# Kernel tuning notes

Hardware: AMD Instinct MI355X
Metric: run time of the kernel (lower is better)

The kernel has to match this reference:

```python
import jax, jax.numpy as jnp
import numpy as np

RENDER_STEP = 0.005
N_FREQS = 6

def pos_enc(x):
    # x: [N,3] -> [N, 3 + 2*N_FREQS*3]
    freqs = (2.0 ** jnp.arange(N_FREQS, dtype=x.dtype)) * jnp.pi
    xb = x[:, None, :] * freqs[:, None]            # [N,F,3]
    enc = jnp.concatenate([jnp.sin(xb), jnp.cos(xb)], axis=-1).reshape(x.shape[0], -1)
    return jnp.concatenate([x, enc], axis=-1)

def geom_fwd(points, Wg0, bg0, Wg1, bg1, Wg2, bg2):
    h = jax.nn.relu(pos_enc(points) @ Wg0 + bg0)
    h = jax.nn.relu(h @ Wg1 + bg1)
    return h @ Wg2 + bg2                           # [N,16]; ch0 = sdf, full vec = features


def setup_inputs() -> dict:
    key = jax.random.key(0)
    ks = jax.random.split(key, 12)
    n_rays, n_samples = 16384, 524288
    sc = lambda fan_in: 1.0 / np.sqrt(fan_in)
    inp = {
        'rays_o': jax.random.normal(ks[0], (n_rays, 3), jnp.float32) * 0.5,
        'rays_d': jax.random.normal(ks[1], (n_rays, 3), jnp.float32),
        'ray_indices': jnp.sort(jax.random.randint(ks[2], (n_samples,), 0, n_rays, jnp.int32)),
        't_starts': jax.random.uniform(ks[3], (n_samples, 1), jnp.float32),
        'random_points': jax.random.normal(ks[4], (1024, 3), jnp.float32),
        's_var': jnp.ones((1,), jnp.float32),
        'Wg0': jax.random.normal(ks[5], (39, 256), jnp.float32) * sc(39),
        'bg0': jnp.zeros((256,), jnp.float32),
        'Wg1': jax.random.normal(ks[6], (256, 256), jnp.float32) * sc(256),
        'bg1': jnp.zeros((256,), jnp.float32),
        'Wg2': jax.random.normal(ks[7], (256, 16), jnp.float32) * sc(256),
        'bg2': jnp.zeros((16,), jnp.float32),
        'Wc0': jax.random.normal(ks[8], (25, 256), jnp.float32) * sc(25),
        'bc0': jnp.zeros((256,), jnp.float32),
        'Wc1': jax.random.normal(ks[9], (256, 3), jnp.float32) * sc(256),
        'bc1': jnp.zeros((3,), jnp.float32),
    }
    return inp


def reference(rays_o, rays_d, ray_indices, t_starts, random_points, s_var,
              Wg0, bg0, Wg1, bg1, Wg2, bg2, Wc0, bc0, Wc1, bc1):
    n_rays = rays_o.shape[0]
    rays_d = rays_d / (jnp.linalg.norm(rays_d, axis=-1, keepdims=True) + 1e-10)

    midpoints = t_starts + RENDER_STEP * 0.5       # [N,1]
    t_intervals = RENDER_STEP
    t_origins = rays_o[ray_indices]                # gather [N,3]
    t_dirs = rays_d[ray_indices]
    points = t_origins + t_dirs * midpoints        # [N,3]

    # SDF network forward + analytic gradient wrt points (one fwd + one bwd)
    out, vjp_fn = jax.vjp(lambda p: geom_fwd(p, Wg0, bg0, Wg1, bg1, Wg2, bg2), points)
    sdf = out[:, 0]                                # [N]
    feats = out                                    # [N,16]
    cot = jnp.zeros_like(out).at[:, 0].set(1.0)
    grad = vjp_fn(cot)[0]                          # dSDF/dpoints [N,3]
    normal = grad / (jnp.linalg.norm(grad, axis=-1, keepdims=True) + 1e-10)

    # color network: dirs + feats + points + normal -> rgb
    cin = jnp.concatenate([t_dirs, feats, points, normal], axis=-1)   # [N,25]
    rgbs = jax.nn.sigmoid(jax.nn.relu(cin @ Wc0 + bc0) @ Wc1 + bc1)   # [N,3]

    # get_alpha (cos_anneal_ratio = 1.0)
    inv_s = jnp.clip(jnp.exp(s_var[0]), 1e-6, 1e6)
    dSDF_dt = jnp.sum(grad * t_dirs, axis=-1, keepdims=True)
    dSDF_dt = -jax.nn.relu(-dSDF_dt)
    cdf = jax.nn.sigmoid(inv_s * sdf[:, None])
    rho = jnp.maximum(inv_s * (cdf - 1.0) * dSDF_dt, 0.0)
    alpha = 1.0 - jnp.exp(-rho * t_intervals)      # [N,1]

    # render_weight_from_alpha: per-ray exclusive cumprod of (1-alpha), log-space
    a = jnp.clip(alpha[:, 0], 0.0, 1.0 - 1e-7)
    loga = jnp.log1p(-a)
    E = jnp.cumsum(loga) - loga                    # exclusive cumsum
    starts = jnp.clip(jnp.searchsorted(ray_indices, jnp.arange(n_rays, dtype=ray_indices.dtype)),
                      0, a.shape[0] - 1)           # first sample idx per ray
    trans = jnp.exp(E - E[starts][ray_indices])    # per-ray transmittance
    weights = (a * trans)[:, None]                 # [N,1]

    seg = lambda v: jax.ops.segment_sum(weights * v, ray_indices, num_segments=n_rays)
    opacity = jax.ops.segment_sum(weights, ray_indices, num_segments=n_rays)  # [R,1]
    depth = seg(midpoints)
    pixels_color = seg(rgbs)
    pixels_normal = seg(normal)
    pixels_normal = pixels_normal / (jnp.linalg.norm(pixels_normal, axis=-1, keepdims=True) + 1e-10)

    random_sdfs = geom_fwd(random_points, Wg0, bg0, Wg1, bg1, Wg2, bg2)[:, :1]
    return (pixels_color, pixels_normal, opacity, depth, weights, sdf, random_sdfs)
```

## Files before the change

### kernel.cpp

```cpp
#include <hip/hip_runtime.h>
#include <math.h>


#define TILE 32
#define NTHREADS 512
#define LDP 264
#define LDE 56
#define LDCIN 40
#define PI_F 3.14159265358979323846f

typedef _Float16 half8 __attribute__((ext_vector_type(8)));
typedef float f32x4 __attribute__((ext_vector_type(4)));
typedef float f32x16 __attribute__((ext_vector_type(16)));

struct alignas(16) SMemK2 {
    _Float16 a0h[TILE * LDP];
    _Float16 a0l[TILE * LDP];
    _Float16 a1h[TILE * LDP];
    _Float16 a1l[TILE * LDP];
    _Float16 ench[TILE * LDE];
    _Float16 encl[TILE * LDE];
    float feats[TILE * 16];
    float red1 [TILE * 16];
    float pts [TILE * 4];
    float dirs[TILE * 4];
    float nrm [TILE * 4];
};

__device__ __forceinline__ void splitst(float v, _Float16* ph, _Float16* pl) {
    _Float16 h = (_Float16)v;
    *ph = h;
    *pl = (_Float16)(v - (float)h);
}

__device__ __forceinline__ f32x16 zero16() {
    f32x16 z;
#pragma unroll
    for (int i = 0; i < 16; ++i) z[i] = 0.f;
    return z;
}

template<int KITERS, bool BIAS, bool RELU, bool AMASK, bool CMASK, bool WLO>
__device__ __forceinline__ void gemm32(
    const _Float16* Ah, const _Float16* Al, const int lda,
    const _Float16* __restrict__ Bp, const float* __restrict__ bias,
    _Float16* Ch, _Float16* Cl, const int ldc,
    const int lane, const int nt)
{
    f32x16 acc0 = zero16(), acc1 = zero16();
    const int row  = lane & 31;
    const int koff = (lane >> 5) * 8;
    const _Float16* ahb = Ah + row * lda + koff;
    const _Float16* alb = Al + row * lda + koff;
    const _Float16* bbase = Bp + ((size_t)nt * KITERS * 64 + lane) * 16;

    half8 ax[2], ay[2];
    half8 bh[3], bl[3];
    ax[0] = *(const half8*)ahb;
    if (!AMASK) ay[0] = *(const half8*)alb;
    bh[0] = *(const half8*)bbase;
    if (!AMASK) bl[0] = *(const half8*)(bbase + 8);
    if (KITERS > 1) {
        bh[1] = *(const half8*)(bbase + 1024);
        if (!AMASK) bl[1] = *(const half8*)(bbase + 1024 + 8);
    }

#pragma unroll
    for (int kit = 0; kit < KITERS; ++kit) {
        const int ac = kit & 1, an = ac ^ 1;
        const int bc = kit % 3;
        if (kit + 1 < KITERS) {
            ax[an] = *(const half8*)(ahb + (kit + 1) * 16);
            if (!AMASK) ay[an] = *(const half8*)(alb + (kit + 1) * 16);
        }
        if (kit + 2 < KITERS) {
            const int bn = (kit + 2) % 3;
            const _Float16* bp = bbase + (size_t)(kit + 2) * 1024;
            bh[bn] = *(const half8*)bp;
            if (!AMASK) bl[bn] = *(const half8*)(bp + 8);
        }
        f32x16& acc = ac ? acc1 : acc0;
        if (AMASK) {
            half8 m;
#pragma unroll
            for (int j = 0; j < 8; ++j) {
                _Float16 t = ax[ac][j] * (_Float16)16384.f;
                m[j] = (t < (_Float16)1.f) ? t : (_Float16)1.f;
            }
            __builtin_amdgcn_s_setprio(1);
            acc = __builtin_amdgcn_mfma_f32_32x32x16_f16(m, bh[bc], acc, 0, 0, 0);
            __builtin_amdgcn_s_setprio(0);
        } else {
            __builtin_amdgcn_s_setprio(1);
            acc = __builtin_amdgcn_mfma_f32_32x32x16_f16(ay[ac], bh[bc], acc, 0, 0, 0);
            acc = __builtin_amdgcn_mfma_f32_32x32x16_f16(ax[ac], bl[bc], acc, 0, 0, 0);
            acc = __builtin_amdgcn_mfma_f32_32x32x16_f16(ax[ac], bh[bc], acc, 0, 0, 0);
            __builtin_amdgcn_s_setprio(0);
        }
    }
    const int col = lane & 31;
    const int rb  = (lane >> 5) * 4;
    const int jc  = nt * 32 + col;
    const float bs = BIAS ? bias[jc] : 0.f;
#pragma unroll
    for (int r = 0; r < 16; ++r) {
        const int srow = (r & 3) + 8 * (r >> 2) + rb;
        float v = acc0[r] + acc1[r] + bs;
        if (RELU) v = (v > 0.f) ? fmaxf(v, 1e-4f) : 0.f;
        if (CMASK) { if (!((float)Ch[srow * ldc + jc] > 0.f)) v = 0.f; }
        _Float16 h = (_Float16)v;
        Ch[srow * ldc + jc] = h;
        if (WLO) Cl[srow * ldc + jc] = (_Float16)(v - (float)h);
    }
}

template<int KITERS>
__device__ __forceinline__ void gemm16(
    const _Float16* Ah, const _Float16* Al, const int lda,
    const _Float16* __restrict__ Bp,
    _Float16* Ch, _Float16* Cl, const int ldc,
    const int lane, const int mt, const int ntbase)
{
    f32x4 acc0 = (f32x4){0.f,0.f,0.f,0.f}, acc1 = (f32x4){0.f,0.f,0.f,0.f};
    const int m  = mt * 16 + (lane & 15);
    const int q8 = (lane >> 4) * 8;
    const _Float16* ahb = Ah + m * lda + q8;
    const _Float16* alb = Al + m * lda + q8;
    const _Float16* bbase = Bp + ((size_t)ntbase * KITERS * 64 + lane) * 16;

    half8 ax[2], ay[2], bh[3], bl[3];
    ax[0] = *(const half8*)ahb;
    ay[0] = *(const half8*)alb;
    bh[0] = *(const half8*)bbase;
    bl[0] = *(const half8*)(bbase + 8);
    if (KITERS > 1) {
        bh[1] = *(const half8*)(bbase + 1024);
        bl[1] = *(const half8*)(bbase + 1024 + 8);
    }
#pragma unroll
    for (int kit = 0; kit < KITERS; ++kit) {
        const int ac = kit & 1, an = ac ^ 1;
        const int bc = kit % 3;
        if (kit + 1 < KITERS) {
            ax[an] = *(const half8*)(ahb + (kit + 1) * 32);
            ay[an] = *(const half8*)(alb + (kit + 1) * 32);
        }
        if (kit + 2 < KITERS) {
            const int bn = (kit + 2) % 3;
            const _Float16* bp = bbase + (size_t)(kit + 2) * 1024;
            bh[bn] = *(const half8*)bp;
            bl[bn] = *(const half8*)(bp + 8);
        }
        f32x4& acc = ac ? acc1 : acc0;
        __builtin_amdgcn_s_setprio(1);
        acc = __builtin_amdgcn_mfma_f32_16x16x32_f16(ay[ac], bh[bc], acc, 0, 0, 0);
        acc = __builtin_amdgcn_mfma_f32_16x16x32_f16(ax[ac], bl[bc], acc, 0, 0, 0);
        acc = __builtin_amdgcn_mfma_f32_16x16x32_f16(ax[ac], bh[bc], acc, 0, 0, 0);
        __builtin_amdgcn_s_setprio(0);
    }
    const int col = lane & 15, q = lane >> 4;
    const int j = ntbase * 16 + col;
#pragma unroll
    for (int r = 0; r < 4; ++r) {
        const int s = mt * 16 + q * 4 + r;
        float v = acc0[r] + acc1[r];
        _Float16 h = (_Float16)v;
        Ch[s * ldc + j] = h;
        Cl[s * ldc + j] = (_Float16)(v - (float)h);
    }
}

__device__ __forceinline__ void kpartial16(
    const _Float16* Ah, const _Float16* Al,
    const _Float16* __restrict__ Bp,
    float* red0, float* red1, const int lane, const int w)
{
    const int mt = w & 1, ks = w >> 1;
    const int m  = mt * 16 + (lane & 15);
    const int q8 = (lane >> 4) * 8;
    const _Float16* ahb = Ah + m * LDP + q8 + ks * 128;
    const _Float16* alb = Al + m * LDP + q8 + ks * 128;
    const _Float16* bbase = Bp + ((size_t)(ks * 4) * 64 + lane) * 16;
    f32x4 acc0 = (f32x4){0.f,0.f,0.f,0.f}, acc1 = (f32x4){0.f,0.f,0.f,0.f};
#pragma unroll
    for (int kit = 0; kit < 4; ++kit) {
        half8 a = *(const half8*)(ahb + kit * 32);
        half8 y = *(const half8*)(alb + kit * 32);
        const _Float16* bp = bbase + (size_t)kit * 1024;
        half8 bh = *(const half8*)bp;
        half8 bl = *(const half8*)(bp + 8);
        f32x4& acc = (kit & 1) ? acc1 : acc0;
        __builtin_amdgcn_s_setprio(1);
        acc = __builtin_amdgcn_mfma_f32_16x16x32_f16(y, bh, acc, 0, 0, 0);
        acc = __builtin_amdgcn_mfma_f32_16x16x32_f16(a, bl, acc, 0, 0, 0);
        acc = __builtin_amdgcn_mfma_f32_16x16x32_f16(a, bh, acc, 0, 0, 0);
        __builtin_amdgcn_s_setprio(0);
    }
    float* red = ks ? red1 : red0;
    const int col = lane & 15, q = lane >> 4;
#pragma unroll
    for (int r = 0; r < 4; ++r)
        red[(mt * 16 + q * 4 + r) * 16 + col] += acc0[r] + acc1[r];
}

__global__ __launch_bounds__(256) void k0_pack(
    const float* __restrict__ Wg0, const float* __restrict__ Wg1,
    const float* __restrict__ Wg2, const float* __restrict__ Wc0,
    const float* __restrict__ Wc1,
    _Float16* __restrict__ Wg0p, _Float16* __restrict__ Wg1p,
    _Float16* __restrict__ Wg1Tp, _Float16* __restrict__ Wg0Tp,
    _Float16* __restrict__ Wc0p, _Float16* __restrict__ Wg2p,
    _Float16* __restrict__ Wc1p)
{
    int gid = blockIdx.x * 256 + threadIdx.x;
    if (gid >= 176128) return;
    int idx, kiters, mode;
    _Float16* dst;
    if      (gid <  12288) { idx = gid;          kiters = 3;  dst = Wg0p;  mode = 0; }
    else if (gid <  77824) { idx = gid -  12288; kiters = 16; dst = Wg1p;  mode = 1; }
    else if (gid < 143360) { idx = gid -  77824; kiters = 16; dst = Wg1Tp; mode = 2; }
    else if (gid < 159744) { idx = gid - 143360; kiters = 8;  dst = Wg0Tp; mode = 3; }
    else if (gid < 167936) { idx = gid - 159744; kiters = 2;  dst = Wc0p;  mode = 4; }
    else if (gid < 172032) { idx = gid - 167936; kiters = 8;  dst = Wg2p;  mode = 5; }
    else                   { idx = gid - 172032; kiters = 8;  dst = Wc1p;  mode = 6; }
    const bool p32 = (mode == 0 || mode == 1 || mode == 2 || mode == 4);
    int j = idx & 7, lane = (idx >> 3) & 63, rest = idx >> 9;
    int kit = rest % kiters, nt = rest / kiters;
    int k, n;
    if (p32) { k = kit * 16 + ((lane >> 5) << 3) + j; n = (nt << 5) + (lane & 31); }
    else     { k = kit * 32 + ((lane >> 4) << 3) + j; n = (nt << 4) + (lane & 15); }
    float val = 0.f;
    switch (mode) {
        case 0: val = (k < 39) ? Wg0[k * 256 + n] : 0.f; break;
        case 1: val = Wg1[k * 256 + n]; break;
        case 2: val = Wg1[n * 256 + k] * Wg2[k * 16]; break;
        case 3: val = (n < 39) ? Wg0[n * 256 + k] : 0.f; break;
        case 4: val = (k < 25) ? Wc0[k * 256 + n] : 0.f; break;
        case 5: val = Wg2[k * 16 + n]; break;
        case 6: val = (n < 3) ? Wc1[k * 3 + n] : 0.f; break;
    }
    _Float16 h = (_Float16)val;
    _Float16 l = (_Float16)(val - (float)h);
    int off = ((nt * kiters + kit) * 64 + lane) * 16 + j;
    dst[off] = h;
    dst[off + 8] = l;
}

__global__ __launch_bounds__(512, 4) void k2_mlp(
    const float* __restrict__ rays_o, const float* __restrict__ rays_d,
    const int*   __restrict__ ray_idx, const float* __restrict__ t_starts,
    const float* __restrict__ s_var,
    const float* __restrict__ bg0, const float* __restrict__ bg1,
    const float* __restrict__ bg2,
    const float* __restrict__ bc0, const float* __restrict__ bc1,
    const _Float16* __restrict__ Wg0p, const _Float16* __restrict__ Wg1p,
    const _Float16* __restrict__ Wg1Tp, const _Float16* __restrict__ Wg0Tp,
    const _Float16* __restrict__ Wc0p, const _Float16* __restrict__ Wg2p,
    const _Float16* __restrict__ Wc1p,
    float* __restrict__ out_sdf, float* __restrict__ ws_a,
    float* __restrict__ ws_rgb, float* __restrict__ ws_nrm,
    int Nsamp)
{
    __shared__ SMemK2 sm;
    const int tid = threadIdx.x;
    const int lane = tid & 63;
    const int w = tid >> 6;
    const int n0 = blockIdx.x * TILE;

    for (int i = tid; i < TILE * 16; i += NTHREADS) {
        sm.feats[i] = bg2[i & 15];
        sm.red1[i] = 0.f;
    }
    if (tid < TILE) {
        int n = n0 + tid; if (n >= Nsamp) n = Nsamp - 1;
        int ri = ray_idx[n];
        float dx = rays_d[ri * 3 + 0], dy = rays_d[ri * 3 + 1], dz = rays_d[ri * 3 + 2];
        float inv = 1.f / (sqrtf(dx * dx + dy * dy + dz * dz) + 1e-10f);
        dx *= inv; dy *= inv; dz *= inv;
        float mid = t_starts[n] + 0.0025f;
        sm.dirs[tid * 4 + 0] = dx; sm.dirs[tid * 4 + 1] = dy; sm.dirs[tid * 4 + 2] = dz;
        float px = rays_o[ri * 3 + 0] + dx * mid;
        float py = rays_o[ri * 3 + 1] + dy * mid;
        float pz = rays_o[ri * 3 + 2] + dz * mid;
        sm.pts[tid * 4 + 0] = px; sm.pts[tid * 4 + 1] = py; sm.pts[tid * 4 + 2] = pz;
        splitst(px, &sm.ench[tid * LDE + 0], &sm.encl[tid * LDE + 0]);
        splitst(py, &sm.ench[tid * LDE + 1], &sm.encl[tid * LDE + 1]);
        splitst(pz, &sm.ench[tid * LDE + 2], &sm.encl[tid * LDE + 2]);
    }
    __syncthreads();

    for (int i = tid; i < TILE * 3; i += NTHREADS) {
        int s = i & 31;
        int d = i >> 5;
        float x = sm.pts[s * 4 + d];
        float a = PI_F * x;
        float sv = sinf(a), cv = cosf(a);
#pragma unroll
        for (int f = 0; f < 6; ++f) {
            splitst(sv, &sm.ench[s * LDE + 3 + f * 6 + d],     &sm.encl[s * LDE + 3 + f * 6 + d]);
            splitst(cv, &sm.ench[s * LDE + 3 + f * 6 + 3 + d], &sm.encl[s * LDE + 3 + f * 6 + 3 + d]);
            float s2 = 2.f * sv * cv;
            float c2 = 1.f - 2.f * sv * sv;
            sv = s2; cv = c2;
        }
    }
    for (int i = tid; i < TILE * 9; i += NTHREADS) {
        int s = i / 9, c = 39 + (i - s * 9);
        sm.ench[s * LDE + c] = (_Float16)0.f;
        sm.encl[s * LDE + c] = (_Float16)0.f;
    }
    __syncthreads();

    gemm32<3, true, true, false, false, true>(sm.ench, sm.encl, LDE,
                                              Wg0p, bg0, sm.a0h, sm.a0l, LDP, lane, w);
    __syncthreads();

    gemm32<16, true, true, false, false, true>(sm.a0h, sm.a0l, LDP,
                                               Wg1p, bg1, sm.a1h, sm.a1l, LDP, lane, w);
    __syncthreads();

    if (w < 4)
        kpartial16(sm.a1h, sm.a1l, Wg2p, sm.feats, sm.red1, lane, w);

    gemm32<16, false, false, true, true, true>(sm.a1h, sm.a1l, LDP,
                                               Wg1Tp, nullptr, sm.a0h, sm.a0l, LDP, lane, w);
    __syncthreads();

    if (w < 6)
        gemm16<8>(sm.a0h, sm.a0l, LDP, Wg0Tp,
                  sm.a1h, sm.a1l, LDP, lane, w & 1, w >> 1);
    __syncthreads();

    if (tid < TILE) {
        int s = tid;
        float g[3];
#pragma unroll
        for (int d = 0; d < 3; ++d)
            g[d] = (float)sm.a1h[s * LDP + d] + (float)sm.a1l[s * LDP + d];
#pragma unroll
        for (int f = 0; f < 6; ++f) {
            float freq = PI_F * (float)(1 << f);
#pragma unroll
            for (int d = 0; d < 3; ++d) {
                int cs = 3 + f * 6 + d, cc = cs + 3;
                float gs = (float)sm.a1h[s * LDP + cs] + (float)sm.a1l[s * LDP + cs];
                float gc = (float)sm.a1h[s * LDP + cc] + (float)sm.a1l[s * LDP + cc];
                float sv = (float)sm.ench[s * LDE + cs] + (float)sm.encl[s * LDE + cs];
                float cv = (float)sm.ench[s * LDE + cc] + (float)sm.encl[s * LDE + cc];
                g[d] += freq * (gs * cv - gc * sv);
            }
        }
        float gl = sqrtf(g[0] * g[0] + g[1] * g[1] + g[2] * g[2]);
        float invl = 1.f / (gl + 1e-10f);
        float nx = g[0] * invl, ny = g[1] * invl, nz = g[2] * invl;
        sm.nrm[s * 4 + 0] = nx; sm.nrm[s * 4 + 1] = ny; sm.nrm[s * 4 + 2] = nz;
        float dx = sm.dirs[s * 4 + 0], dy = sm.dirs[s * 4 + 1], dz = sm.dirs[s * 4 + 2];
        float dsdt = fminf(g[0] * dx + g[1] * dy + g[2] * dz, 0.f);
        float sdf = sm.feats[s * 16 + 0] + sm.red1[s * 16 + 0];
        float inv_s = __expf(s_var[0]);
        inv_s = fminf(fmaxf(inv_s, 1e-6f), 1e6f);
        float cdf = 1.f / (1.f + __expf(-inv_s * sdf));
        float rho = fmaxf(inv_s * (cdf - 1.f) * dsdt, 0.f);
        float alpha = 1.f - __expf(-rho * 0.005f);
        float a = fminf(fmaxf(alpha, 0.f), 1.f - 1e-7f);
        int n = n0 + s;
        if (n < Nsamp) {
            out_sdf[n] = sdf;
            ws_a[n] = a;
            ws_nrm[n * 3 + 0] = nx; ws_nrm[n * 3 + 1] = ny; ws_nrm[n * 3 + 2] = nz;
        }
    }
    __syncthreads();

    _Float16* cinh = sm.a0h;
    _Float16* cinl = sm.a0l;
    for (int i = tid; i < TILE * 32; i += NTHREADS) {
        int s = i >> 5, c = i & 31;
        float v = 0.f;
        if      (c < 3)  v = sm.dirs[s * 4 + c];
        else if (c < 19) v = sm.feats[s * 16 + (c - 3)] + sm.red1[s * 16 + (c - 3)];
        else if (c < 22) v = sm.pts[s * 4 + (c - 19)];
        else if (c < 25) v = sm.nrm[s * 4 + (c - 22)];
        splitst(v, &cinh[s * LDCIN + c], &cinl[s * LDCIN + c]);
    }
    __syncthreads();

    for (int i = tid; i < TILE * 16; i += NTHREADS) {
        sm.feats[i] = ((i & 15) < 3) ? bc1[i & 15] : 0.f;
        sm.red1[i] = 0.f;
    }

    gemm32<2, true, true, false, false, true>(cinh, cinl, LDCIN,
                                              Wc0p, bc0, sm.a1h, sm.a1l, LDP, lane, w);
    __syncthreads();

    if (w < 4)
        kpartial16(sm.a1h, sm.a1l, Wc1p, sm.feats, sm.red1, lane, w);
    __syncthreads();

    if (tid < TILE) {
        int n = n0 + tid;
        if (n < Nsamp) {
#pragma unroll
            for (int c = 0; c < 3; ++c) {
                float z = sm.feats[tid * 16 + c] + sm.red1[tid * 16 + c];
                ws_rgb[n * 3 + c] = 1.f / (1.f + __expf(-z));
            }
        }
    }
}

__global__ void k3_composite(
    const int* __restrict__ ray_idx, const float* __restrict__ t_starts,
    const float* __restrict__ ws_a, const float* __restrict__ ws_rgb,
    const float* __restrict__ ws_nrm,
    float* __restrict__ out_pc, float* __restrict__ out_pn,
    float* __restrict__ out_op, float* __restrict__ out_dp,
    float* __restrict__ out_w, int n_rays, int Nsamp)
{
    int r = blockIdx.x * blockDim.x + threadIdx.x;
    if (r >= n_rays) return;
    int lo = 0, hi = Nsamp;
    while (lo < hi) { int m = (lo + hi) >> 1; if (ray_idx[m] < r) lo = m + 1; else hi = m; }
    int start = lo;
    hi = Nsamp;
    while (lo < hi) { int m = (lo + hi) >> 1; if (ray_idx[m] < r + 1) lo = m + 1; else hi = m; }
    int end = lo;

    float T = 1.f, aco = 0.f, acd = 0.f;
    float c0 = 0.f, c1 = 0.f, c2 = 0.f, nx = 0.f, ny = 0.f, nz = 0.f;
    for (int n = start; n < end; ++n) {
        float a = ws_a[n];
        float wgt = a * T;
        T *= (1.f - a);
        out_w[n] = wgt;
        float mid = t_starts[n] + 0.0025f;
        aco += wgt; acd += wgt * mid;
        c0 += wgt * ws_rgb[n * 3 + 0];
        c1 += wgt * ws_rgb[n * 3 + 1];
        c2 += wgt * ws_rgb[n * 3 + 2];
        nx += wgt * ws_nrm[n * 3 + 0];
        ny += wgt * ws_nrm[n * 3 + 1];
        nz += wgt * ws_nrm[n * 3 + 2];
    }
    out_op[r] = aco;
    out_dp[r] = acd;
    out_pc[r * 3 + 0] = c0; out_pc[r * 3 + 1] = c1; out_pc[r * 3 + 2] = c2;
    float nl = sqrtf(nx * nx + ny * ny + nz * nz);
    float inv = 1.f / (nl + 1e-10f);
    out_pn[r * 3 + 0] = nx * inv; out_pn[r * 3 + 1] = ny * inv; out_pn[r * 3 + 2] = nz * inv;
}

__global__ __launch_bounds__(256) void k4_random(
    const float* __restrict__ pts,
    const float* __restrict__ Wg0, const float* __restrict__ bg0,
    const float* __restrict__ Wg1, const float* __restrict__ bg1,
    const float* __restrict__ Wg2, const float* __restrict__ bg2,
    float* __restrict__ out_rs, int n_rand)
{
    __shared__ float enc[40];
    __shared__ float h[256];
    __shared__ float red[256];
    int b = blockIdx.x;
    if (b >= n_rand) return;
    int tid = threadIdx.x;
    if (tid < 39) {
        int c = tid;
        float v;
        if (c < 3) v = pts[b * 3 + c];
        else {
            int e = c - 3, f = e / 6, r = e - f * 6;
            float freq = PI_F * (float)(1 << f);
            int d = (r < 3) ? r : r - 3;
            float x = pts[b * 3 + d];
            v = (r < 3) ? sinf(freq * x) : cosf(freq * x);
        }
        enc[c] = v;
    }
    __syncthreads();
    {
        float z = bg0[tid];
        for (int m = 0; m < 39; ++m) z += enc[m] * Wg0[m * 256 + tid];
        h[tid] = fmaxf(z, 0.f);
    }
    __syncthreads();
    {
        float z = bg1[tid];
        for (int k = 0; k < 256; ++k) z += h[k] * Wg1[k * 256 + tid];
        float h1 = fmaxf(z, 0.f);
        red[tid] = h1 * Wg2[tid * 16];
    }
    __syncthreads();
    for (int off = 128; off > 0; off >>= 1) {
        if (tid < off) red[tid] += red[tid + off];
        __syncthreads();
    }
    if (tid == 0) out_rs[b] = red[0] + bg2[0];
}

extern "C" void kernel_launch(void* const* d_in, const int* in_sizes, int n_in,
                              void* d_out, int out_size, void* d_ws, size_t ws_size,
                              hipStream_t stream)
{
    const float* rays_o   = (const float*)d_in[0];
    const float* rays_d   = (const float*)d_in[1];
    const int*   ray_idx  = (const int*)  d_in[2];
    const float* t_starts = (const float*)d_in[3];
    const float* rpts     = (const float*)d_in[4];
    const float* s_var    = (const float*)d_in[5];
    const float* Wg0 = (const float*)d_in[6];  const float* bg0 = (const float*)d_in[7];
    const float* Wg1 = (const float*)d_in[8];  const float* bg1 = (const float*)d_in[9];
    const float* Wg2 = (const float*)d_in[10]; const float* bg2 = (const float*)d_in[11];
    const float* Wc0 = (const float*)d_in[12]; const float* bc0 = (const float*)d_in[13];
    const float* Wc1 = (const float*)d_in[14]; const float* bc1 = (const float*)d_in[15];

    const int n_rays = in_sizes[0] / 3;
    const int Ns     = in_sizes[2];
    const int n_rand = in_sizes[4] / 3;

    float* out  = (float*)d_out;
    float* o_pc = out;
    float* o_pn = out + (size_t)3 * n_rays;
    float* o_op = out + (size_t)6 * n_rays;
    float* o_dp = out + (size_t)7 * n_rays;
    float* o_w  = out + (size_t)8 * n_rays;
    float* o_sdf = o_w + Ns;
    float* o_rs  = o_sdf + Ns;

    _Float16* hptr  = (_Float16*)d_ws;
    _Float16* Wg0p  = hptr;
    _Float16* Wg1p  = Wg0p  + 24576;
    _Float16* Wg1Tp = Wg1p  + 131072;
    _Float16* Wg0Tp = Wg1Tp + 131072;
    _Float16* Wc0p  = Wg0Tp + 32768;
    _Float16* Wg2p  = Wc0p  + 16384;
    _Float16* Wc1p  = Wg2p  + 8192;
    float* fbase  = (float*)(hptr + 352256);
    float* ws_a   = fbase;
    float* ws_rgb = ws_a + Ns;
    float* ws_nrm = ws_rgb + (size_t)3 * Ns;

    hipLaunchKernelGGL(k0_pack, dim3(688), dim3(256), 0, stream,
                       Wg0, Wg1, Wg2, Wc0, Wc1,
                       Wg0p, Wg1p, Wg1Tp, Wg0Tp, Wc0p, Wg2p, Wc1p);
    hipLaunchKernelGGL(k2_mlp, dim3((Ns + TILE - 1) / TILE), dim3(NTHREADS), 0, stream,
                       rays_o, rays_d, ray_idx, t_starts, s_var,
                       bg0, bg1, bg2, bc0, bc1,
                       Wg0p, Wg1p, Wg1Tp, Wg0Tp, Wc0p, Wg2p, Wc1p,
                       o_sdf, ws_a, ws_rgb, ws_nrm, Ns);
    hipLaunchKernelGGL(k4_random, dim3(n_rand), dim3(256), 0, stream,
                       rpts, Wg0, bg0, Wg1, bg1, Wg2, bg2, o_rs, n_rand);
    hipLaunchKernelGGL(k3_composite, dim3((n_rays + 255) / 256), dim3(256), 0, stream,
                       ray_idx, t_starts, ws_a, ws_rgb, ws_nrm,
                       o_pc, o_pn, o_op, o_dp, o_w, n_rays, Ns);
}
```

Baseline: 729.4 us.

## Fold random-point SDF into MLP kernel and parallelize compositing per-ray wavefront

Random-point SDF evaluation now runs as extra tiles of the tensor-core MLP kernel, which exit after the SDF head, replacing the separate scalar k4_random kernel. The compositing kernel assigns one 64-lane wavefront per ray and computes transmittance with a shuffle-based prefix product, replacing one serial thread per ray. Points are recomputed directly in the encoding loop and normals are written straight into the color-input tile, which removes one barrier and a shared buffer. The risks are extra redundant gathers, and wasted lanes in the compositing kernel, since rays average about 32 samples and each wavefront still runs two binary searches.

```diff
diff --git a/kernel.cpp b/kernel.cpp
--- a/kernel.cpp
+++ b/kernel.cpp
@@ -24,7 +24,6 @@
     float red1 [TILE * 16];
     float pts [TILE * 4];
     float dirs[TILE * 4];
-    float nrm [TILE * 4];
 };
 
 __device__ __forceinline__ void splitst(float v, _Float16* ph, _Float16* pl) {
@@ -249,7 +248,7 @@
 __global__ __launch_bounds__(512, 4) void k2_mlp(
     const float* __restrict__ rays_o, const float* __restrict__ rays_d,
     const int*   __restrict__ ray_idx, const float* __restrict__ t_starts,
-    const float* __restrict__ s_var,
+    const float* __restrict__ s_var, const float* __restrict__ rpts,
     const float* __restrict__ bg0, const float* __restrict__ bg1,
     const float* __restrict__ bg2,
     const float* __restrict__ bc0, const float* __restrict__ bc1,
@@ -259,19 +258,22 @@
     const _Float16* __restrict__ Wc1p,
     float* __restrict__ out_sdf, float* __restrict__ ws_a,
     float* __restrict__ ws_rgb, float* __restrict__ ws_nrm,
-    int Nsamp)
+    float* __restrict__ out_rs,
+    int Nsamp, int n_rand)
 {
     __shared__ SMemK2 sm;
     const int tid = threadIdx.x;
     const int lane = tid & 63;
     const int w = tid >> 6;
-    const int n0 = blockIdx.x * TILE;
+    const int ntb = (Nsamp + TILE - 1) / TILE;
+    const bool rnd = (int)blockIdx.x >= ntb;
+    const int n0 = (rnd ? (blockIdx.x - ntb) : blockIdx.x) * TILE;
 
     for (int i = tid; i < TILE * 16; i += NTHREADS) {
         sm.feats[i] = bg2[i & 15];
         sm.red1[i] = 0.f;
     }
-    if (tid < TILE) {
+    if (!rnd && tid < TILE) {
         int n = n0 + tid; if (n >= Nsamp) n = Nsamp - 1;
         int ri = ray_idx[n];
         float dx = rays_d[ri * 3 + 0], dy = rays_d[ri * 3 + 1], dz = rays_d[ri * 3 + 2];
@@ -279,20 +281,26 @@
         dx *= inv; dy *= inv; dz *= inv;
         float mid = t_starts[n] + 0.0025f;
         sm.dirs[tid * 4 + 0] = dx; sm.dirs[tid * 4 + 1] = dy; sm.dirs[tid * 4 + 2] = dz;
-        float px = rays_o[ri * 3 + 0] + dx * mid;
-        float py = rays_o[ri * 3 + 1] + dy * mid;
-        float pz = rays_o[ri * 3 + 2] + dz * mid;
-        sm.pts[tid * 4 + 0] = px; sm.pts[tid * 4 + 1] = py; sm.pts[tid * 4 + 2] = pz;
-        splitst(px, &sm.ench[tid * LDE + 0], &sm.encl[tid * LDE + 0]);
-        splitst(py, &sm.ench[tid * LDE + 1], &sm.encl[tid * LDE + 1]);
-        splitst(pz, &sm.ench[tid * LDE + 2], &sm.encl[tid * LDE + 2]);
-    }
-    __syncthreads();
+        sm.pts[tid * 4 + 0] = rays_o[ri * 3 + 0] + dx * mid;
+        sm.pts[tid * 4 + 1] = rays_o[ri * 3 + 1] + dy * mid;
+        sm.pts[tid * 4 + 2] = rays_o[ri * 3 + 2] + dz * mid;
+    }
 
     for (int i = tid; i < TILE * 3; i += NTHREADS) {
         int s = i & 31;
         int d = i >> 5;
-        float x = sm.pts[s * 4 + d];
+        float x;
+        if (rnd) {
+            int n = n0 + s; if (n >= n_rand) n = n_rand - 1;
+            x = rpts[n * 3 + d];
+        } else {
+            int n = n0 + s; if (n >= Nsamp) n = Nsamp - 1;
+            int ri = ray_idx[n];
+            float dx = rays_d[ri * 3 + 0], dy = rays_d[ri * 3 + 1], dz = rays_d[ri * 3 + 2];
+            float inv = 1.f / (sqrtf(dx * dx + dy * dy + dz * dz) + 1e-10f);
+            x = rays_o[ri * 3 + d] + rays_d[ri * 3 + d] * inv * (t_starts[n] + 0.0025f);
+        }
+        splitst(x, &sm.ench[s * LDE + d], &sm.encl[s * LDE + d]);
         float a = PI_F * x;
         float sv = sinf(a), cv = cosf(a);
 #pragma unroll
@@ -322,6 +330,16 @@
     if (w < 4)
         kpartial16(sm.a1h, sm.a1l, Wg2p, sm.feats, sm.red1, lane, w);
 
+    if (rnd) {
+        __syncthreads();
+        if (tid < TILE) {
+            int n = n0 + tid;
+            if (n < n_rand)
+                out_rs[n] = sm.feats[tid * 16] + sm.red1[tid * 16];
+        }
+        return;
+    }
+
     gemm32<16, false, false, true, true, true>(sm.a1h, sm.a1l, LDP,
                                                Wg1Tp, nullptr, sm.a0h, sm.a0l, LDP, lane, w);
     __syncthreads();
@@ -331,6 +349,8 @@
                   sm.a1h, sm.a1l, LDP, lane, w & 1, w >> 1);
     __syncthreads();
 
+    _Float16* cinh = sm.a0h;
+    _Float16* cinl = sm.a0l;
     if (tid < TILE) {
         int s = tid;
         float g[3];
@@ -353,7 +373,9 @@
         float gl = sqrtf(g[0] * g[0] + g[1] * g[1] + g[2] * g[2]);
         float invl = 1.f / (gl + 1e-10f);
         float nx = g[0] * invl, ny = g[1] * invl, nz = g[2] * invl;
-        sm.nrm[s * 4 + 0] = nx; sm.nrm[s * 4 + 1] = ny; sm.nrm[s * 4 + 2] = nz;
+        splitst(nx, &cinh[s * LDCIN + 22], &cinl[s * LDCIN + 22]);
+        splitst(ny, &cinh[s * LDCIN + 23], &cinl[s * LDCIN + 23]);
+        splitst(nz, &cinh[s * LDCIN + 24], &cinl[s * LDCIN + 24]);
         float dx = sm.dirs[s * 4 + 0], dy = sm.dirs[s * 4 + 1], dz = sm.dirs[s * 4 + 2];
         float dsdt = fminf(g[0] * dx + g[1] * dy + g[2] * dz, 0.f);
         float sdf = sm.feats[s * 16 + 0] + sm.red1[s * 16 + 0];
@@ -370,17 +392,13 @@
             ws_nrm[n * 3 + 0] = nx; ws_nrm[n * 3 + 1] = ny; ws_nrm[n * 3 + 2] = nz;
         }
     }
-    __syncthreads();
-
-    _Float16* cinh = sm.a0h;
-    _Float16* cinl = sm.a0l;
     for (int i = tid; i < TILE * 32; i += NTHREADS) {
         int s = i >> 5, c = i & 31;
+        if (c >= 22 && c < 25) continue;
         float v = 0.f;
         if      (c < 3)  v = sm.dirs[s * 4 + c];
         else if (c < 19) v = sm.feats[s * 16 + (c - 3)] + sm.red1[s * 16 + (c - 3)];
         else if (c < 22) v = sm.pts[s * 4 + (c - 19)];
-        else if (c < 25) v = sm.nrm[s * 4 + (c - 22)];
         splitst(v, &cinh[s * LDCIN + c], &cinl[s * LDCIN + c]);
     }
     __syncthreads();
@@ -410,7 +428,7 @@
     }
 }
 
-__global__ void k3_composite(
+__global__ __launch_bounds__(256) void k3_composite(
     const int* __restrict__ ray_idx, const float* __restrict__ t_starts,
     const float* __restrict__ ws_a, const float* __restrict__ ws_rgb,
     const float* __restrict__ ws_nrm,
@@ -418,84 +436,60 @@
     float* __restrict__ out_op, float* __restrict__ out_dp,
     float* __restrict__ out_w, int n_rays, int Nsamp)
 {
-    int r = blockIdx.x * blockDim.x + threadIdx.x;
+    const int lane = threadIdx.x & 63;
+    const int r = (blockIdx.x * blockDim.x + threadIdx.x) >> 6;
     if (r >= n_rays) return;
+
     int lo = 0, hi = Nsamp;
     while (lo < hi) { int m = (lo + hi) >> 1; if (ray_idx[m] < r) lo = m + 1; else hi = m; }
-    int start = lo;
+    const int start = lo;
     hi = Nsamp;
     while (lo < hi) { int m = (lo + hi) >> 1; if (ray_idx[m] < r + 1) lo = m + 1; else hi = m; }
-    int end = lo;
+    const int end = lo;
 
     float T = 1.f, aco = 0.f, acd = 0.f;
     float c0 = 0.f, c1 = 0.f, c2 = 0.f, nx = 0.f, ny = 0.f, nz = 0.f;
-    for (int n = start; n < end; ++n) {
-        float a = ws_a[n];
-        float wgt = a * T;
-        T *= (1.f - a);
-        out_w[n] = wgt;
-        float mid = t_starts[n] + 0.0025f;
-        aco += wgt; acd += wgt * mid;
-        c0 += wgt * ws_rgb[n * 3 + 0];
-        c1 += wgt * ws_rgb[n * 3 + 1];
-        c2 += wgt * ws_rgb[n * 3 + 2];
-        nx += wgt * ws_nrm[n * 3 + 0];
-        ny += wgt * ws_nrm[n * 3 + 1];
-        nz += wgt * ws_nrm[n * 3 + 2];
-    }
-    out_op[r] = aco;
-    out_dp[r] = acd;
-    out_pc[r * 3 + 0] = c0; out_pc[r * 3 + 1] = c1; out_pc[r * 3 + 2] = c2;
-    float nl = sqrtf(nx * nx + ny * ny + nz * nz);
-    float inv = 1.f / (nl + 1e-10f);
-    out_pn[r * 3 + 0] = nx * inv; out_pn[r * 3 + 1] = ny * inv; out_pn[r * 3 + 2] = nz * inv;
-}
-
-__global__ __launch_bounds__(256) void k4_random(
-    const float* __restrict__ pts,
-    const float* __restrict__ Wg0, const float* __restrict__ bg0,
-    const float* __restrict__ Wg1, const float* __restrict__ bg1,
-    const float* __restrict__ Wg2, const float* __restrict__ bg2,
-    float* __restrict__ out_rs, int n_rand)
-{
-    __shared__ float enc[40];
-    __shared__ float h[256];
-    __shared__ float red[256];
-    int b = blockIdx.x;
-    if (b >= n_rand) return;
-    int tid = threadIdx.x;
-    if (tid < 39) {
-        int c = tid;
-        float v;
-        if (c < 3) v = pts[b * 3 + c];
-        else {
-            int e = c - 3, f = e / 6, r = e - f * 6;
-            float freq = PI_F * (float)(1 << f);
-            int d = (r < 3) ? r : r - 3;
-            float x = pts[b * 3 + d];
-            v = (r < 3) ? sinf(freq * x) : cosf(freq * x);
-        }
-        enc[c] = v;
-    }
-    __syncthreads();
-    {
-        float z = bg0[tid];
-        for (int m = 0; m < 39; ++m) z += enc[m] * Wg0[m * 256 + tid];
-        h[tid] = fmaxf(z, 0.f);
-    }
-    __syncthreads();
-    {
-        float z = bg1[tid];
-        for (int k = 0; k < 256; ++k) z += h[k] * Wg1[k * 256 + tid];
-        float h1 = fmaxf(z, 0.f);
-        red[tid] = h1 * Wg2[tid * 16];
-    }
-    __syncthreads();
-    for (int off = 128; off > 0; off >>= 1) {
-        if (tid < off) red[tid] += red[tid + off];
-        __syncthreads();
-    }
-    if (tid == 0) out_rs[b] = red[0] + bg2[0];
+    for (int base = start; base < end; base += 64) {
+        const int n = base + lane;
+        const bool act = n < end;
+        float a = act ? ws_a[n] : 0.f;
+        float p = 1.f - a;
+#pragma unroll
+        for (int off = 1; off < 64; off <<= 1) {
+            float t = __shfl_up(p, off);
+            if (lane >= off) p *= t;
+        }
+        float e = __shfl_up(p, 1);
+        if (lane == 0) e = 1.f;
+        float wgt = a * T * e;
+        if (act) {
+            out_w[n] = wgt;
+            float mid = t_starts[n] + 0.0025f;
+            aco += wgt; acd += wgt * mid;
+            c0 += wgt * ws_rgb[n * 3 + 0];
+            c1 += wgt * ws_rgb[n * 3 + 1];
+            c2 += wgt * ws_rgb[n * 3 + 2];
+            nx += wgt * ws_nrm[n * 3 + 0];
+            ny += wgt * ws_nrm[n * 3 + 1];
+            nz += wgt * ws_nrm[n * 3 + 2];
+        }
+        T *= __shfl(p, 63);
+    }
+#pragma unroll
+    for (int off = 32; off > 0; off >>= 1) {
+        aco += __shfl_xor(aco, off); acd += __shfl_xor(acd, off);
+        c0  += __shfl_xor(c0,  off); c1  += __shfl_xor(c1,  off);
+        c2  += __shfl_xor(c2,  off); nx  += __shfl_xor(nx,  off);
+        ny  += __shfl_xor(ny,  off); nz  += __shfl_xor(nz,  off);
+    }
+    if (lane == 0) {
+        out_op[r] = aco;
+        out_dp[r] = acd;
+        out_pc[r * 3 + 0] = c0; out_pc[r * 3 + 1] = c1; out_pc[r * 3 + 2] = c2;
+        float nl = sqrtf(nx * nx + ny * ny + nz * nz);
+        float inv = 1.f / (nl + 1e-10f);
+        out_pn[r * 3 + 0] = nx * inv; out_pn[r * 3 + 1] = ny * inv; out_pn[r * 3 + 2] = nz * inv;
+    }
 }
 
 extern "C" void kernel_launch(void* const* d_in, const int* in_sizes, int n_in,
@@ -540,17 +534,18 @@
     float* ws_rgb = ws_a + Ns;
     float* ws_nrm = ws_rgb + (size_t)3 * Ns;
 
+    const int ntb = (Ns + TILE - 1) / TILE;
+    const int nrb = (n_rand + TILE - 1) / TILE;
+
     hipLaunchKernelGGL(k0_pack, dim3(688), dim3(256), 0, stream,
                        Wg0, Wg1, Wg2, Wc0, Wc1,
                        Wg0p, Wg1p, Wg1Tp, Wg0Tp, Wc0p, Wg2p, Wc1p);
-    hipLaunchKernelGGL(k2_mlp, dim3((Ns + TILE - 1) / TILE), dim3(NTHREADS), 0, stream,
-                       rays_o, rays_d, ray_idx, t_starts, s_var,
+    hipLaunchKernelGGL(k2_mlp, dim3(ntb + nrb), dim3(NTHREADS), 0, stream,
+                       rays_o, rays_d, ray_idx, t_starts, s_var, rpts,
                        bg0, bg1, bg2, bc0, bc1,
                        Wg0p, Wg1p, Wg1Tp, Wg0Tp, Wc0p, Wg2p, Wc1p,
-                       o_sdf, ws_a, ws_rgb, ws_nrm, Ns);
-    hipLaunchKernelGGL(k4_random, dim3(n_rand), dim3(256), 0, stream,
-                       rpts, Wg0, bg0, Wg1, bg1, Wg2, bg2, o_rs, n_rand);
-    hipLaunchKernelGGL(k3_composite, dim3((n_rays + 255) / 256), dim3(256), 0, stream,
+                       o_sdf, ws_a, ws_rgb, ws_nrm, o_rs, Ns, n_rand);
+    hipLaunchKernelGGL(k3_composite, dim3((n_rays * 64 + 255) / 256), dim3(256), 0, stream,
                        ray_idx, t_starts, ws_a, ws_rgb, ws_nrm,
                        o_pc, o_pn, o_op, o_dp, o_w, n_rays, Ns);
 }
```

Measured after the change: 680.7 us. 6.7% less time.
